# Kernel optimization log

Measured on AMD Instinct MI355X. Metric: run time of the kernel, lower is better.

The kernel has to match this reference:

```python
import jax, jax.numpy as jnp
import numpy as np
from jax import lax

# LRN hyperparameters (from module __init__)
K = 2.0
KERNEL = 5
ALPHA = 1e-4
BETA = 0.75
PAD = KERNEL // 2


def setup_inputs() -> dict:
    key = jax.random.key(0)
    x = jax.random.normal(key, (16, 96, 224, 224), dtype=jnp.float32)
    return {"x": x}


def reference(x) -> jnp.ndarray:
    # Spatial local response norm: per-channel k x k box sum of squares
    # (equivalent to Unfold(kernel, pad=kernel//2) -> view -> square -> sum over window).
    sq = x * x
    ssq = lax.reduce_window(
        sq,
        jnp.float32(0.0),
        lax.add,
        window_dimensions=(1, 1, KERNEL, KERNEL),
        window_strides=(1, 1, 1, 1),
        padding=((0, 0), (0, 0), (PAD, PAD), (PAD, PAD)),
    )
    denom = (K + ALPHA * ssq) ** BETA
    return x / denom
```

## Files before the change

kernel.cpp:

```cpp
#include <hip/hip_runtime.h>


typedef float f4 __attribute__((ext_vector_type(4)));

#define LRN_H 224
#define LRN_W 224
#define LRN_WQ 56
#define LRN_R 8
#define LRN_JOBS_PER_PLANE (LRN_H / LRN_R)
#define LRN_PLANE (LRN_H * LRN_W)

__device__ __forceinline__ f4 lrn_ld(const float* __restrict__ p) {
    return *(const f4*)p;
}

__device__ __forceinline__ f4 lrn_hsum(f4 xl, f4 xc, f4 xr,
                                       float mL, float mR, float mV) {
    float a  = xl[2] * xl[2] * mL;
    float b  = xl[3] * xl[3] * mL;
    float c0 = xc[0] * xc[0];
    float c1 = xc[1] * xc[1];
    float c2 = xc[2] * xc[2];
    float c3 = xc[3] * xc[3];
    float d0 = xr[0] * xr[0] * mR;
    float d1 = xr[1] * xr[1] * mR;
    float t = c1 + c2;
    f4 r;
    r[0] = (a + b + c0 + t) * mV;
    r[1] = (b + c0 + t + c3) * mV;
    r[2] = (c0 + t + c3 + d0) * mV;
    r[3] = (t + c3 + d0 + d1) * mV;
    return r;
}

__global__ __launch_bounds__(256, 4) void LocalResponseNorm_17420387352942_kernel(
        const float* __restrict__ x, float* __restrict__ out) {
    const int q    = threadIdx.x & 63;
    const int wave = threadIdx.x >> 6;
    const int job  = blockIdx.x * 4 + wave;
    const int plane = job / LRN_JOBS_PER_PLANE;
    const int slab  = job - plane * LRN_JOBS_PER_PLANE;
    const int h0    = slab * LRN_R;

    const int qe = min(q, LRN_WQ - 1);
    const float* __restrict__ px = x   + (size_t)plane * LRN_PLANE + (qe << 2);
    float* __restrict__       po = out + (size_t)plane * LRN_PLANE + (qe << 2);

    const float mL = (qe > 0)          ? 1.0f : 0.0f;
    const float mR = (qe < LRN_WQ - 1) ? 1.0f : 0.0f;
    const int offL = (qe > 0)          ? -4 : 0;
    const int offR = (qe < LRN_WQ - 1) ?  4 : 0;
    const bool wr  = (q < LRN_WQ);

    f4 rs[LRN_R + 4];
    f4 cen[LRN_R];

#pragma unroll
    for (int r = 0; r < LRN_R + 4; ++r) {
        const int row = h0 + r - 2;
        float mV = 1.0f;
        int rc = row;
        if (r < 2)      { mV = (row >= 0)     ? 1.0f : 0.0f; rc = max(row, 0); }
        else if (r > 9) { mV = (row < LRN_H)  ? 1.0f : 0.0f; rc = min(row, LRN_H - 1); }
        const float* rp = px + rc * LRN_W;
        f4 xc = lrn_ld(rp);
        f4 xl = lrn_ld(rp + offL);
        f4 xr = lrn_ld(rp + offR);
        rs[r] = lrn_hsum(xl, xc, xr, mL, mR, mV);
        if (r >= 2 && r < 2 + LRN_R) cen[r - 2] = xc;
    }

#pragma unroll
    for (int i = 0; i < LRN_R; ++i) {
        f4 s = rs[i] + rs[i + 1] + rs[i + 2] + rs[i + 3] + rs[i + 4];
        f4 o;
#pragma unroll
        for (int j = 0; j < 4; ++j) {
            float d  = fmaf(1e-4f, s[j], 2.0f);
            float rsq = __builtin_amdgcn_rsqf(d);
            o[j] = cen[i][j] * rsq * __builtin_amdgcn_sqrtf(rsq);
        }
        if (wr) __builtin_nontemporal_store(o, (f4*)(po + (h0 + i) * LRN_W));
    }
}

extern "C" void kernel_launch(void* const* d_in, const int* in_sizes, int n_in,
                              void* d_out, int out_size, void* d_ws, size_t ws_size,
                              hipStream_t stream) {
    const float* x = (const float*)d_in[0];
    float* out = (float*)d_out;
    dim3 block(256, 1, 1);
    dim3 grid(43008 / 4, 1, 1);
    LocalResponseNorm_17420387352942_kernel<<<grid, block, 0, stream>>>(x, out);
}
```

Before: 496.0 us.

## Use wave shuffles for horizontal neighbors and halve rows per wave

Replaces the left and right neighbor vector loads with cross-lane shuffles of the squared values, so each row is loaded once instead of three times. Rows per wave drop from 8 to 4 and the grid doubles, with occupancy hint raised to 6. This cuts redundant cache traffic and register pressure, at the cost of more vertical halo reloads (8 rows read per 4 output instead of 12 per 8).

```diff
diff --git a/kernel.cpp b/kernel.cpp
--- a/kernel.cpp
+++ b/kernel.cpp
@@ -6,79 +6,77 @@
 #define LRN_H 224
 #define LRN_W 224
 #define LRN_WQ 56
-#define LRN_R 8
-#define LRN_JOBS_PER_PLANE (LRN_H / LRN_R)
+#define LRN_R 4
+#define LRN_IN (LRN_R + 4)
+#define LRN_SLABS (LRN_H / LRN_R)
 #define LRN_PLANE (LRN_H * LRN_W)
 
-__device__ __forceinline__ f4 lrn_ld(const float* __restrict__ p) {
-    return *(const f4*)p;
-}
-
-__device__ __forceinline__ f4 lrn_hsum(f4 xl, f4 xc, f4 xr,
-                                       float mL, float mR, float mV) {
-    float a  = xl[2] * xl[2] * mL;
-    float b  = xl[3] * xl[3] * mL;
-    float c0 = xc[0] * xc[0];
-    float c1 = xc[1] * xc[1];
-    float c2 = xc[2] * xc[2];
-    float c3 = xc[3] * xc[3];
-    float d0 = xr[0] * xr[0] * mR;
-    float d1 = xr[1] * xr[1] * mR;
-    float t = c1 + c2;
-    f4 r;
-    r[0] = (a + b + c0 + t) * mV;
-    r[1] = (b + c0 + t + c3) * mV;
-    r[2] = (c0 + t + c3 + d0) * mV;
-    r[3] = (t + c3 + d0 + d1) * mV;
-    return r;
-}
-
-__global__ __launch_bounds__(256, 4) void LocalResponseNorm_17420387352942_kernel(
+__global__ __launch_bounds__(256, 6) void LocalResponseNorm_17420387352942_kernel(
         const float* __restrict__ x, float* __restrict__ out) {
     const int q    = threadIdx.x & 63;
     const int wave = threadIdx.x >> 6;
     const int job  = blockIdx.x * 4 + wave;
-    const int plane = job / LRN_JOBS_PER_PLANE;
-    const int slab  = job - plane * LRN_JOBS_PER_PLANE;
+    const int plane = job / LRN_SLABS;
+    const int slab  = job - plane * LRN_SLABS;
     const int h0    = slab * LRN_R;
 
     const int qe = min(q, LRN_WQ - 1);
     const float* __restrict__ px = x   + (size_t)plane * LRN_PLANE + (qe << 2);
     float* __restrict__       po = out + (size_t)plane * LRN_PLANE + (qe << 2);
 
-    const float mL = (qe > 0)          ? 1.0f : 0.0f;
-    const float mR = (qe < LRN_WQ - 1) ? 1.0f : 0.0f;
-    const int offL = (qe > 0)          ? -4 : 0;
-    const int offR = (qe < LRN_WQ - 1) ?  4 : 0;
+    const bool okL = (qe > 0);
+    const bool okR = (qe < LRN_WQ - 1);
     const bool wr  = (q < LRN_WQ);
 
-    f4 rs[LRN_R + 4];
-    f4 cen[LRN_R];
+    f4 X[LRN_IN];
+#pragma unroll
+    for (int r = 0; r < LRN_IN; ++r) {
+        const int row = h0 + r - 2;
+        const int rc  = min(max(row, 0), LRN_H - 1);
+        X[r] = *(const f4*)(px + rc * LRN_W);
+    }
+
+    f4 acc[LRN_R];
+#pragma unroll
+    for (int i = 0; i < LRN_R; ++i) acc[i] = (f4){0.f, 0.f, 0.f, 0.f};
 
 #pragma unroll
-    for (int r = 0; r < LRN_R + 4; ++r) {
+    for (int r = 0; r < LRN_IN; ++r) {
         const int row = h0 + r - 2;
-        float mV = 1.0f;
-        int rc = row;
-        if (r < 2)      { mV = (row >= 0)     ? 1.0f : 0.0f; rc = max(row, 0); }
-        else if (r > 9) { mV = (row < LRN_H)  ? 1.0f : 0.0f; rc = min(row, LRN_H - 1); }
-        const float* rp = px + rc * LRN_W;
-        f4 xc = lrn_ld(rp);
-        f4 xl = lrn_ld(rp + offL);
-        f4 xr = lrn_ld(rp + offR);
-        rs[r] = lrn_hsum(xl, xc, xr, mL, mR, mV);
-        if (r >= 2 && r < 2 + LRN_R) cen[r - 2] = xc;
+        const float mV = (row >= 0 && row < LRN_H) ? 1.0f : 0.0f;
+        f4 sq = X[r] * X[r];
+        sq *= mV;
+
+        float a  = __shfl_up(sq[2], 1);
+        float b  = __shfl_up(sq[3], 1);
+        float d0 = __shfl_down(sq[0], 1);
+        float d1 = __shfl_down(sq[1], 1);
+        a  = okL ? a  : 0.0f;
+        b  = okL ? b  : 0.0f;
+        d0 = okR ? d0 : 0.0f;
+        d1 = okR ? d1 : 0.0f;
+
+        float t = sq[1] + sq[2];
+        f4 rs;
+        rs[0] = a + b + sq[0] + t;
+        rs[1] = b + sq[0] + t + sq[3];
+        rs[2] = sq[0] + t + sq[3] + d0;
+        rs[3] = t + sq[3] + d0 + d1;
+
+#pragma unroll
+        for (int i = 0; i < LRN_R; ++i) {
+            if (i <= r && r <= i + 4) acc[i] += rs;
+        }
     }
 
 #pragma unroll
     for (int i = 0; i < LRN_R; ++i) {
-        f4 s = rs[i] + rs[i + 1] + rs[i + 2] + rs[i + 3] + rs[i + 4];
         f4 o;
 #pragma unroll
         for (int j = 0; j < 4; ++j) {
-            float d  = fmaf(1e-4f, s[j], 2.0f);
+            float d   = fmaf(1e-4f, acc[i][j], 2.0f);
             float rsq = __builtin_amdgcn_rsqf(d);
-            o[j] = cen[i][j] * rsq * __builtin_amdgcn_sqrtf(rsq);
+            o[j] = X[i + 2][j] * rsq * __builtin_amdgcn_sqrtf(rsq);
         }
         if (wr) __builtin_nontemporal_store(o, (f4*)(po + (h0 + i) * LRN_W));
     }
@@ -90,6 +88,6 @@
     const float* x = (const float*)d_in[0];
     float* out = (float*)d_out;
     dim3 block(256, 1, 1);
-    dim3 grid(43008 / 4, 1, 1);
+    dim3 grid(86016 / 4, 1, 1);
     LocalResponseNorm_17420387352942_kernel<<<grid, block, 0, stream>>>(x, out);
 }
```

Result: slower. 512.0 us (+3.2%).
